# Performance work log

Hardware: AMD Instinct MI355X
Metric: run time of the kernel (lower is better)

## Reference

```python
import jax, jax.numpy as jnp
import numpy as np

N_FFT = 256
HOP = 64
HS = 126  # window hop in STFT frames (hard-coded in original)


def _stft(x):
    # torch.stft(center=True, pad_mode='reflect', window=None -> rectangular,
    # onesided=True, normalized=False). x: [B, N] -> [B, T, F] (time-major,
    # matching the module's permute(0,1,3,2)).
    pad = N_FFT // 2
    xp = jnp.pad(x, ((0, 0), (pad, pad)), mode='reflect')
    T = x.shape[-1] // HOP + 1
    idx = jnp.arange(T)[:, None] * HOP + jnp.arange(N_FFT)[None, :]  # [T, n_fft]
    frames = xp[:, idx]  # [B, T, n_fft]
    return jnp.fft.rfft(frames, axis=-1)  # [B, T, F=129]


def _spec_match(mix, aux):
    mixS = _stft(mix[:, 0, :])  # [B, Tm, F] complex
    auxS = _stft(aux[:, 0, :])  # [B, Ta, F] complex
    B, Tm, F = mixS.shape
    Ta = auxS.shape[1]
    length = (Ta - Tm) // HS
    pad = HS - (Ta - Tm) % HS
    auxS = jnp.pad(auxS, ((0, 0), (0, pad), (0, 0)))
    # All sliding windows at once: [B, W, Tm, F]
    W = length + 2
    widx = jnp.arange(W)[:, None] * HS + jnp.arange(Tm)[None, :]  # [W, Tm]
    wins = auxS[:, widx, :]  # [B, W, Tm, F]
    # Real part of complex cosine similarity, elementwise
    m = mixS[:, None]  # [B, 1, Tm, F]
    sim = (m.real * wins.real + m.imag * wins.imag) / (jnp.abs(m) * jnp.abs(wins))
    flat = sim.reshape(B, W, -1)
    n = flat.shape[-1]
    # torch.median = lower median; torch.median returns NaN if any NaN present
    srt = jnp.sort(flat, axis=-1)
    med = srt[..., (n - 1) // 2]
    med = jnp.where(jnp.isnan(flat).any(-1), -jnp.inf, med)
    best = jnp.argmax(med, axis=1)  # [B], first max like Python max()
    sel = jnp.take_along_axis(wins, best[:, None, None, None], axis=1)  # [B,1,Tm,F]
    return jnp.concatenate([sel.real, sel.imag], axis=1)  # [B, 2, Tm, F]


def setup_inputs() -> dict:
    key = jax.random.key(0)
    k1, k2 = jax.random.split(key)
    mix = jax.random.normal(k1, (8, 1, 65536), dtype=jnp.float32)
    aux = jax.random.normal(k2, (8, 1, 262144), dtype=jnp.float32)
    return {"mix": mix, "aux": aux}


def reference(mix, aux):
    return _spec_match(mix, aux)
```

## Files before the change

### kernel.cpp

```cpp
#include <hip/hip_runtime.h>
#include <math.h>

constexpr int NFFT  = 256;
constexpr int HOP   = 64;
constexpr int NBIN  = 129;
constexpr int NB    = 8;
constexpr int LMIX  = 65536;
constexpr int LAUX  = 262144;
constexpr int TM    = 1025;
constexpr int TA    = 4097;
constexpr int TROWS = 4175;
constexpr int HS    = 126;
constexpr int W     = 26;
constexpr int NJOBS = NB * W;
constexpr int NVAL  = TM * NBIN;
constexpr int KMED  = (NVAL - 1) / 2;
constexpr int CHUNKS = 8;
constexpr int NBA   = 1024;
constexpr int FPB   = 8;
constexpr int MIXBLKS = (TM + FPB - 1) / FPB;
constexpr int AUXBLKS = (TROWS + FPB - 1) / FPB;
constexpr int GFPB  = 4;
constexpr int GBLKS = (TM + GFPB - 1) / GFPB;

constexpr size_t MIXN_OFF  = 0;
constexpr size_t MIXN_BYTES = (size_t)NB * TM * NBIN * sizeof(float2);
constexpr size_t AUXN_OFF  = MIXN_OFF + MIXN_BYTES;
constexpr size_t AUXN_BYTES = (size_t)NB * TROWS * NBIN * sizeof(float2);
constexpr size_t HIST_OFF  = AUXN_OFF + AUXN_BYTES;
constexpr size_t HIST_BYTES = (size_t)NJOBS * CHUNKS * NBA * 4;
constexpr size_t CAND_OFF  = HIST_OFF + HIST_BYTES;
constexpr size_t CAND_BYTES = (size_t)NJOBS * NVAL * 4;
constexpr size_t NAN_OFF   = CAND_OFF + CAND_BYTES;
constexpr size_t NAN_BYTES = (size_t)NJOBS * CHUNKS * 4;
constexpr size_t NCAND_OFF = NAN_OFF + NAN_BYTES;
constexpr size_t SELBIN_OFF= NCAND_OFF + 832;
constexpr size_t KREM_OFF  = SELBIN_OFF + 832;
constexpr size_t MED_OFF   = KREM_OFF + 832;

constexpr float TWOPI_N = (float)(-2.0 * 3.14159265358979323846 / 256.0);

__device__ __forceinline__ float2 twiddle(int k) {
    float s, c;
    sincosf(TWOPI_N * (float)k, &s, &c);
    return make_float2(c, s);
}

__global__ void stft_all(const float* __restrict__ mix, const float* __restrict__ aux,
                         float2* __restrict__ mixN, float2* __restrict__ auxN,
                         unsigned* __restrict__ ncand)
{
    constexpr int NX = 64 * (FPB - 1) + NFFT;
    __shared__ float  xs[NX];
    __shared__ float2 Yl[FPB][16][16];
    __shared__ float2 tw256[256];
    __shared__ float2 cis16[16];

    const int tid  = threadIdx.x;
    const int wgid = blockIdx.x;
    const int b    = wgid & 7;
    const int t    = wgid >> 3;
    const bool isMix = t < MIXBLKS;
    const int f0 = (isMix ? t : t - MIXBLKS) * FPB;
    const int L       = isMix ? LMIX : LAUX;
    const int Tframes = isMix ? TM : TA;
    const int Trows   = isMix ? TM : TROWS;
    const float* x    = isMix ? mix : aux;
    float2* out       = isMix ? mixN : auxN;

    if (wgid == 0 && tid < NJOBS) ncand[tid] = 0u;

    tw256[tid] = twiddle(tid);
    if (tid < 16) cis16[tid] = twiddle(16 * tid);

    for (int i = tid; i < NX; i += 256) {
        int j = f0 * HOP + i - 128;
        if (j < 0) j = -j;
        if (j >= L) j = 2 * L - 2 - j;
        xs[i] = x[(size_t)b * L + j];
    }
    __syncthreads();

    const int n1 = (tid >> 4) & 15;
    const int r  = tid & 15;
    {
        float reA[FPB], imA[FPB];
        #pragma unroll
        for (int f = 0; f < FPB; ++f) { reA[f] = 0.f; imA[f] = 0.f; }
        int idx = 0;
        #pragma unroll
        for (int n2 = 0; n2 < 16; ++n2) {
            float2 tv = cis16[idx];
            #pragma unroll
            for (int f = 0; f < FPB; ++f) {
                float v = xs[f * HOP + n1 + 16 * n2];
                reA[f] = fmaf(v, tv.x, reA[f]);
                imA[f] = fmaf(v, tv.y, imA[f]);
            }
            idx = (idx + r) & 15;
        }
        #pragma unroll
        for (int f = 0; f < FPB; ++f) Yl[f][n1][r] = make_float2(reA[f], imA[f]);
    }
    __syncthreads();

    const float QNAN = __int_as_float(0x7FC00000);
    auto emit = [&](int fr, int k, float ar, float ai) {
        if (fr >= Trows) return;
        float2 o;
        if (fr < Tframes) {
            float inv = rsqrtf(ar * ar + ai * ai);
            o = make_float2(ar * inv, ai * inv);
        } else {
            o = make_float2(QNAN, QNAN);
        }
        out[((size_t)b * Trows + fr) * NBIN + k] = o;
    };

    #pragma unroll 1
    for (int p = 0; p < 2; ++p) {
        const int jjA = tid + 512 * p;
        const int jjB = jjA + 256;
        const int fA = jjA / NBIN, kA = jjA - fA * NBIN;
        const int fB = jjB / NBIN, kB = jjB - fB * NBIN;
        const float2 dkA = tw256[kA];
        const float2 dkB = tw256[kB];
        float trA = 1.f, tiA = 0.f, arA = 0.f, aiA = 0.f;
        float trB = 1.f, tiB = 0.f, arB = 0.f, aiB = 0.f;
        #pragma unroll
        for (int s = 0; s < 16; ++s) {
            float2 yA = Yl[fA][s][kA & 15];
            float2 yB = Yl[fB][s][kB & 15];
            arA = fmaf(trA, yA.x, arA); arA = fmaf(-tiA, yA.y, arA);
            aiA = fmaf(trA, yA.y, aiA); aiA = fmaf( tiA, yA.x, aiA);
            arB = fmaf(trB, yB.x, arB); arB = fmaf(-tiB, yB.y, arB);
            aiB = fmaf(trB, yB.y, aiB); aiB = fmaf( tiB, yB.x, aiB);
            float nrA = trA * dkA.x - tiA * dkA.y;
            tiA = fmaf(trA, dkA.y, tiA * dkA.x); trA = nrA;
            float nrB = trB * dkB.x - tiB * dkB.y;
            tiB = fmaf(trB, dkB.y, tiB * dkB.x); trB = nrB;
        }
        emit(f0 + fA, kA, arA, aiA);
        emit(f0 + fB, kB, arB, aiB);
    }
    if (tid < FPB * NBIN - 1024) {
        const int jj = 1024 + tid;
        const int f = jj / NBIN, k = jj - f * NBIN;
        const float2 dk = tw256[k];
        float tr = 1.f, ti = 0.f, ar = 0.f, ai = 0.f;
        #pragma unroll
        for (int s = 0; s < 16; ++s) {
            float2 y = Yl[f][s][k & 15];
            ar = fmaf(tr, y.x, ar); ar = fmaf(-ti, y.y, ar);
            ai = fmaf(tr, y.y, ai); ai = fmaf( ti, y.x, ai);
            float nr = tr * dk.x - ti * dk.y;
            ti = fmaf(tr, dk.y, ti * dk.x); tr = nr;
        }
        emit(f0 + f, k, ar, ai);
    }
}

__device__ __forceinline__ unsigned flip_key(float s) {
    unsigned u = __float_as_uint(s);
    return (u & 0x80000000u) ? ~u : (u | 0x80000000u);
}
__device__ __forceinline__ unsigned qbin(float s) {
    if (!(s == s)) return (unsigned)(NBA - 1);
    int bq = (int)floorf(fmaf(s, 512.f, 512.f));
    bq = max(0, min(NBA - 1, bq));
    return (unsigned)bq;
}

template<int PER>
__device__ __forceinline__ void rank_find(const unsigned (&bins)[PER], unsigned target,
                                          unsigned& out_bin, unsigned& out_rem)
{
    __shared__ unsigned wtot[4];
    __shared__ unsigned result[2];
    const int tid  = threadIdx.x;
    const int lane = tid & 63;
    const int wid  = tid >> 6;

    unsigned st = 0;
    #pragma unroll
    for (int i = 0; i < PER; ++i) st += bins[i];

    unsigned inc = st;
    #pragma unroll
    for (int d = 1; d < 64; d <<= 1) {
        unsigned v = __shfl_up(inc, d);
        if (lane >= d) inc += v;
    }
    if (lane == 63) wtot[wid] = inc;
    __syncthreads();

    unsigned wbase = 0;
    for (int wme = 0; wme < wid; ++wme) wbase += wtot[wme];
    unsigned ex = wbase + inc - st;
    if ((ex <= target) && (target < ex + st)) {
        unsigned cum = ex;
        #pragma unroll
        for (int i = 0; i < PER; ++i) {
            if (cum + bins[i] > target) {
                result[0] = (unsigned)(tid * PER + i);
                result[1] = target - cum;
                break;
            }
            cum += bins[i];
        }
    }
    __syncthreads();
    out_bin = result[0];
    out_rem = result[1];
}

__global__ void sim_hist(const float2* __restrict__ mixN, const float2* __restrict__ auxN,
                         unsigned* __restrict__ hist, unsigned* __restrict__ nanCnt)
{
    constexpr int NCOPY   = 4;
    constexpr int HSTRIDE = NBA + 1;
    __shared__ unsigned lh[NCOPY * HSTRIDE];
    __shared__ unsigned bnan;
    const int tid   = threadIdx.x;
    const int wgid  = blockIdx.x;
    const int b     = wgid & 7;
    const int rest  = wgid >> 3;
    const int w     = rest / CHUNKS;
    const int chunk = rest - w * CHUNKS;
    const int job   = b * W + w;
    unsigned* lhc = lh + ((tid >> 4) & (NCOPY - 1)) * HSTRIDE;

    for (int i = tid; i < NCOPY * HSTRIDE; i += 256) lh[i] = 0;
    if (tid == 0) bnan = 0;
    __syncthreads();

    unsigned localnan = 0;
    const float2* mrow = mixN + (size_t)b * TM * NBIN;
    const float2* arow = auxN + ((size_t)b * TROWS + (size_t)w * HS) * NBIN;

    const int pad = b & 1;
    const int lim = pad + ((NVAL - pad) & ~1);

    for (int i = pad + (chunk * 256 + tid) * 2; i < lim; i += CHUNKS * 512) {
        float4 mv = *reinterpret_cast<const float4*>(mrow + i);
        float4 av = *reinterpret_cast<const float4*>(arow + i);
        float s0 = fmaf(mv.x, av.x, mv.y * av.y);
        float s1 = fmaf(mv.z, av.z, mv.w * av.w);
        if (!(s0 == s0)) localnan++;
        if (!(s1 == s1)) localnan++;
        atomicAdd(&lhc[qbin(s0)], 1u);
        atomicAdd(&lhc[qbin(s1)], 1u);
    }
    if (chunk == 0 && tid == 0) {
        int ie = pad ? 0 : NVAL - 1;
        float2 m = mrow[ie];
        float2 a = arow[ie];
        float s = fmaf(m.x, a.x, m.y * a.y);
        if (!(s == s)) localnan++;
        atomicAdd(&lhc[qbin(s)], 1u);
    }
    if (localnan) atomicAdd(&bnan, localnan);
    __syncthreads();

    unsigned* gh = hist + ((size_t)job * CHUNKS + chunk) * NBA;
    for (int i = tid; i < NBA; i += 256)
        gh[i] = lh[i] + lh[HSTRIDE + i] + lh[2 * HSTRIDE + i] + lh[3 * HSTRIDE + i];
    if (tid == 0) nanCnt[job * CHUNKS + chunk] = bnan;
}

__global__ void scan_bins(const unsigned* __restrict__ hist, unsigned* __restrict__ selbin,
                          unsigned* __restrict__ krem)
{
    constexpr int PER = NBA / 256;
    const int tid  = threadIdx.x;
    const int wgid = blockIdx.x;
    const int job  = (wgid & 7) * W + (wgid >> 3);
    const unsigned* h = hist + (size_t)job * CHUNKS * NBA;

    unsigned bins[PER];
    #pragma unroll
    for (int i = 0; i < PER; ++i) {
        unsigned v = 0;
        int bin = tid * PER + i;
        #pragma unroll
        for (int c = 0; c < CHUNKS; ++c) v += h[(size_t)c * NBA + bin];
        bins[i] = v;
    }
    unsigned sb, rem;
    rank_find<PER>(bins, (unsigned)KMED, sb, rem);
    if (tid == 0) { selbin[job] = sb; krem[job] = rem; }
}

__global__ void sim_compact(const float2* __restrict__ mixN, const float2* __restrict__ auxN,
                            const unsigned* __restrict__ selbin, unsigned* __restrict__ cand,
                            unsigned* __restrict__ ncand)
{
    const int tid   = threadIdx.x;
    const int wgid  = blockIdx.x;
    const int b     = wgid & 7;
    const int rest  = wgid >> 3;
    const int w     = rest / CHUNKS;
    const int chunk = rest - w * CHUNKS;
    const int job   = b * W + w;
    const unsigned sb = selbin[job];

    unsigned* candj  = cand + (size_t)job * NVAL;
    unsigned* ncandj = ncand + job;
    const int lane = tid & 63;

    const float2* mrow = mixN + (size_t)b * TM * NBIN;
    const float2* arow = auxN + ((size_t)b * TROWS + (size_t)w * HS) * NBIN;

    const int pad = b & 1;
    const int lim = pad + ((NVAL - pad) & ~1);

    for (int i = pad + (chunk * 256 + tid) * 2; i < lim; i += CHUNKS * 512) {
        float4 mv = *reinterpret_cast<const float4*>(mrow + i);
        float4 av = *reinterpret_cast<const float4*>(arow + i);
        float sv[2];
        sv[0] = fmaf(mv.x, av.x, mv.y * av.y);
        sv[1] = fmaf(mv.z, av.z, mv.w * av.w);
        #pragma unroll
        for (int u = 0; u < 2; ++u) {
            bool pred = (qbin(sv[u]) == sb);
            unsigned long long m = __ballot(pred);
            if (m) {
                int leader = __ffsll(m) - 1;
                unsigned base = 0;
                if (lane == leader) base = atomicAdd(ncandj, (unsigned)__popcll(m));
                base = (unsigned)__shfl((int)base, leader);
                if (pred) candj[base + __popcll(m & ((1ull << lane) - 1ull))] = flip_key(sv[u]);
            }
        }
    }
    if (chunk == 0 && tid == 0) {
        int ie = pad ? 0 : NVAL - 1;
        float2 m = mrow[ie];
        float2 a = arow[ie];
        float s = fmaf(m.x, a.x, m.y * a.y);
        if (qbin(s) == sb) {
            unsigned idx = atomicAdd(ncandj, 1u);
            candj[idx] = flip_key(s);
        }
    }
}

__global__ void select_kernel(const unsigned* __restrict__ cand, const unsigned* __restrict__ ncand,
                              const unsigned* __restrict__ krem, const unsigned* __restrict__ nanCnt,
                              float* __restrict__ med)
{
    __shared__ unsigned h[2048];
    const int wgid = blockIdx.x;
    const int job  = (wgid & 7) * W + (wgid >> 3);
    const int tid  = threadIdx.x;
    const unsigned* c = cand + (size_t)job * NVAL;
    const unsigned n = ncand[job];
    unsigned pref = 0, tgt = krem[job];

    for (int ph = 0; ph < 3; ++ph) {
        for (int i = tid; i < 2048; i += 256) h[i] = 0;
        __syncthreads();
        for (unsigned i = tid; i < n; i += 256) {
            unsigned k = c[i];
            if (ph == 0) atomicAdd(&h[k >> 21], 1u);
            else if (ph == 1) { if ((k >> 21) == (pref >> 21)) atomicAdd(&h[(k >> 10) & 2047u], 1u); }
            else { if ((k >> 10) == (pref >> 10)) atomicAdd(&h[k & 1023u], 1u); }
        }
        __syncthreads();

        unsigned bins[8];
        #pragma unroll
        for (int i = 0; i < 8; ++i) bins[i] = h[tid * 8 + i];
        unsigned sb, rem;
        rank_find<8>(bins, tgt, sb, rem);

        if (ph == 0)      pref = sb << 21;
        else if (ph == 1) pref |= sb << 10;
        else              pref |= sb;
        tgt = rem;
        __syncthreads();
    }

    if (tid == 0) {
        unsigned nan = 0;
        #pragma unroll
        for (int c2 = 0; c2 < CHUNKS; ++c2) nan += nanCnt[job * CHUNKS + c2];
        unsigned key = pref;
        unsigned u = (key & 0x80000000u) ? (key ^ 0x80000000u) : ~key;
        med[job] = (nan > 0u) ? -INFINITY : __uint_as_float(u);
    }
}

__global__ void gather_stft(const float* __restrict__ x, const float* __restrict__ med,
                            float* __restrict__ out)
{
    constexpr int NX = 64 * (GFPB - 1) + NFFT;
    __shared__ float  xs[NX];
    __shared__ float2 Yl[GFPB][16][16];
    __shared__ float2 tw256[256];
    __shared__ float2 cis16[16];
    __shared__ int sh_best;

    const int tid  = threadIdx.x;
    const int wgid = blockIdx.x;
    const int b    = wgid & 7;
    const int t0   = (wgid >> 3) * GFPB;

    if (tid == 0) {
        float mx = -INFINITY; int bi = 0;
        for (int w = 0; w < W; ++w) {
            float v = med[b * W + w];
            if (v > mx) { mx = v; bi = w; }
        }
        sh_best = bi;
    }
    tw256[tid] = twiddle(tid);
    if (tid < 16) cis16[tid] = twiddle(16 * tid);
    __syncthreads();

    const int fr0 = sh_best * HS + t0;

    for (int i = tid; i < NX; i += 256) {
        int j = fr0 * HOP + i - 128;
        if (j < 0) j = -j;
        if (j >= LAUX) j = 2 * LAUX - 2 - j;
        j = max(0, min(LAUX - 1, j));
        xs[i] = x[(size_t)b * LAUX + j];
    }
    __syncthreads();

    const int n1 = (tid >> 4) & 15;
    const int r  = tid & 15;
    {
        float reA[GFPB], imA[GFPB];
        #pragma unroll
        for (int f = 0; f < GFPB; ++f) { reA[f] = 0.f; imA[f] = 0.f; }
        int idx = 0;
        #pragma unroll
        for (int n2 = 0; n2 < 16; ++n2) {
            float2 tv = cis16[idx];
            #pragma unroll
            for (int f = 0; f < GFPB; ++f) {
                float v = xs[f * HOP + n1 + 16 * n2];
                reA[f] = fmaf(v, tv.x, reA[f]);
                imA[f] = fmaf(v, tv.y, imA[f]);
            }
            idx = (idx + r) & 15;
        }
        #pragma unroll
        for (int f = 0; f < GFPB; ++f) Yl[f][n1][r] = make_float2(reA[f], imA[f]);
    }
    __syncthreads();

    auto dotask = [&](int jj) {
        const int f = jj / NBIN, k = jj - f * NBIN;
        const int tt = t0 + f;
        if (tt >= TM) return;
        float ar = 0.f, ai = 0.f;
        if (fr0 + f < TA) {
            const float2 dk = tw256[k];
            float tr = 1.f, ti = 0.f;
            #pragma unroll
            for (int s = 0; s < 16; ++s) {
                float2 y = Yl[f][s][k & 15];
                ar = fmaf(tr, y.x, ar); ar = fmaf(-ti, y.y, ar);
                ai = fmaf(tr, y.y, ai); ai = fmaf( ti, y.x, ai);
                float nr = tr * dk.x - ti * dk.y;
                ti = fmaf(tr, dk.y, ti * dk.x); tr = nr;
            }
        }
        size_t o = (size_t)tt * NBIN + k;
        out[(size_t)(b * 2 + 0) * NVAL + o] = ar;
        out[(size_t)(b * 2 + 1) * NVAL + o] = ai;
    };
    dotask(tid);
    dotask(tid + 256);
    if (tid < GFPB * NBIN - 512) dotask(512 + tid);
}

extern "C" void kernel_launch(void* const* d_in, const int* in_sizes, int n_in,
                              void* d_out, int out_size, void* d_ws, size_t ws_size,
                              hipStream_t stream)
{
    const float* mix = (const float*)d_in[0];
    const float* aux = (const float*)d_in[1];
    float* out = (float*)d_out;
    char* ws = (char*)d_ws;

    float2*   mixN = (float2*)(ws + MIXN_OFF);
    float2*   auxN = (float2*)(ws + AUXN_OFF);
    unsigned* hist = (unsigned*)(ws + HIST_OFF);
    unsigned* cand = (unsigned*)(ws + CAND_OFF);
    unsigned* nanC = (unsigned*)(ws + NAN_OFF);
    unsigned* ncand= (unsigned*)(ws + NCAND_OFF);
    unsigned* selb = (unsigned*)(ws + SELBIN_OFF);
    unsigned* krem = (unsigned*)(ws + KREM_OFF);
    float*    med  = (float*)(ws + MED_OFF);

    stft_all<<<(MIXBLKS + AUXBLKS) * NB, 256, 0, stream>>>(mix, aux, mixN, auxN, ncand);
    sim_hist<<<NJOBS * CHUNKS, 256, 0, stream>>>(mixN, auxN, hist, nanC);
    scan_bins<<<NJOBS, 256, 0, stream>>>(hist, selb, krem);
    sim_compact<<<NJOBS * CHUNKS, 256, 0, stream>>>(mixN, auxN, selb, cand, ncand);
    select_kernel<<<NJOBS, 256, 0, stream>>>(cand, ncand, krem, nanC, med);
    gather_stft<<<GBLKS * NB, 256, 0, stream>>>(aux, med, out);
}
```

Baseline: 122.9 us.

## Cache coarse bin bytes in histogram pass to skip recompute in compaction

The histogram pass now also writes one byte per similarity value holding the coarse bin (bin>>2). The compaction pass reads these bytes eight at a time, uses a SWAR zero-byte test to find possible matches, and only then loads the mix/aux spectra to recompute and check the exact bin. This replaces the full re-read of both complex spectra (16 bytes per element) with a 1-byte-per-element stream plus sparse gathers. It costs an extra byte-array write in sim_hist and adds scattered per-candidate atomics. The gather kernel also doubles frames per block and loops over tasks.

Measured after the change: 126.5 us. +2.9%, slower.

```diff
diff --git a/kernel.cpp b/kernel.cpp
--- a/kernel.cpp
+++ b/kernel.cpp
@@ -14,13 +14,14 @@
 constexpr int W     = 26;
 constexpr int NJOBS = NB * W;
 constexpr int NVAL  = TM * NBIN;
+constexpr int NVALB = 132232;
 constexpr int KMED  = (NVAL - 1) / 2;
 constexpr int CHUNKS = 8;
 constexpr int NBA   = 1024;
 constexpr int FPB   = 8;
 constexpr int MIXBLKS = (TM + FPB - 1) / FPB;
 constexpr int AUXBLKS = (TROWS + FPB - 1) / FPB;
-constexpr int GFPB  = 4;
+constexpr int GFPB  = 8;
 constexpr int GBLKS = (TM + GFPB - 1) / GFPB;
 
 constexpr size_t MIXN_OFF  = 0;
@@ -31,7 +32,9 @@
 constexpr size_t HIST_BYTES = (size_t)NJOBS * CHUNKS * NBA * 4;
 constexpr size_t CAND_OFF  = HIST_OFF + HIST_BYTES;
 constexpr size_t CAND_BYTES = (size_t)NJOBS * NVAL * 4;
-constexpr size_t NAN_OFF   = CAND_OFF + CAND_BYTES;
+constexpr size_t BYTES_OFF = CAND_OFF + CAND_BYTES;
+constexpr size_t BYTES_BYTES = (size_t)NJOBS * NVALB;
+constexpr size_t NAN_OFF   = BYTES_OFF + BYTES_BYTES;
 constexpr size_t NAN_BYTES = (size_t)NJOBS * CHUNKS * 4;
 constexpr size_t NCAND_OFF = NAN_OFF + NAN_BYTES;
 constexpr size_t SELBIN_OFF= NCAND_OFF + 832;
@@ -215,7 +218,8 @@
 }
 
 __global__ void sim_hist(const float2* __restrict__ mixN, const float2* __restrict__ auxN,
-                         unsigned* __restrict__ hist, unsigned* __restrict__ nanCnt)
+                         unsigned* __restrict__ hist, unsigned char* __restrict__ bytes,
+                         unsigned* __restrict__ nanCnt)
 {
     constexpr int NCOPY   = 4;
     constexpr int HSTRIDE = NBA + 1;
@@ -237,6 +241,7 @@
     unsigned localnan = 0;
     const float2* mrow = mixN + (size_t)b * TM * NBIN;
     const float2* arow = auxN + ((size_t)b * TROWS + (size_t)w * HS) * NBIN;
+    unsigned char* bj = bytes + (size_t)job * NVALB;
 
     const int pad = b & 1;
     const int lim = pad + ((NVAL - pad) & ~1);
@@ -248,8 +253,11 @@
         float s1 = fmaf(mv.z, av.z, mv.w * av.w);
         if (!(s0 == s0)) localnan++;
         if (!(s1 == s1)) localnan++;
-        atomicAdd(&lhc[qbin(s0)], 1u);
-        atomicAdd(&lhc[qbin(s1)], 1u);
+        unsigned b0 = qbin(s0), b1 = qbin(s1);
+        atomicAdd(&lhc[b0], 1u);
+        atomicAdd(&lhc[b1], 1u);
+        bj[i]     = (unsigned char)(b0 >> 2);
+        bj[i + 1] = (unsigned char)(b1 >> 2);
     }
     if (chunk == 0 && tid == 0) {
         int ie = pad ? 0 : NVAL - 1;
@@ -257,7 +265,9 @@
         float2 a = arow[ie];
         float s = fmaf(m.x, a.x, m.y * a.y);
         if (!(s == s)) localnan++;
-        atomicAdd(&lhc[qbin(s)], 1u);
+        unsigned be = qbin(s);
+        atomicAdd(&lhc[be], 1u);
+        bj[ie] = (unsigned char)(be >> 2);
     }
     if (localnan) atomicAdd(&bnan, localnan);
     __syncthreads();
@@ -292,6 +302,7 @@
 }
 
 __global__ void sim_compact(const float2* __restrict__ mixN, const float2* __restrict__ auxN,
+                            const unsigned char* __restrict__ bytes,
                             const unsigned* __restrict__ selbin, unsigned* __restrict__ cand,
                             unsigned* __restrict__ ncand)
 {
@@ -303,40 +314,36 @@
     const int chunk = rest - w * CHUNKS;
     const int job   = b * W + w;
     const unsigned sb = selbin[job];
+    const unsigned long long pat = 0x0101010101010101ULL * (unsigned long long)(sb >> 2);
 
     unsigned* candj  = cand + (size_t)job * NVAL;
     unsigned* ncandj = ncand + job;
-    const int lane = tid & 63;
-
     const float2* mrow = mixN + (size_t)b * TM * NBIN;
     const float2* arow = auxN + ((size_t)b * TROWS + (size_t)w * HS) * NBIN;
-
-    const int pad = b & 1;
-    const int lim = pad + ((NVAL - pad) & ~1);
-
-    for (int i = pad + (chunk * 256 + tid) * 2; i < lim; i += CHUNKS * 512) {
-        float4 mv = *reinterpret_cast<const float4*>(mrow + i);
-        float4 av = *reinterpret_cast<const float4*>(arow + i);
-        float sv[2];
-        sv[0] = fmaf(mv.x, av.x, mv.y * av.y);
-        sv[1] = fmaf(mv.z, av.z, mv.w * av.w);
-        #pragma unroll
-        for (int u = 0; u < 2; ++u) {
-            bool pred = (qbin(sv[u]) == sb);
-            unsigned long long m = __ballot(pred);
-            if (m) {
-                int leader = __ffsll(m) - 1;
-                unsigned base = 0;
-                if (lane == leader) base = atomicAdd(ncandj, (unsigned)__popcll(m));
-                base = (unsigned)__shfl((int)base, leader);
-                if (pred) candj[base + __popcll(m & ((1ull << lane) - 1ull))] = flip_key(sv[u]);
+    const unsigned long long* bj8 =
+        reinterpret_cast<const unsigned long long*>(bytes + (size_t)job * NVALB);
+
+    constexpr int NGRP = NVAL / 8;
+    for (int g = chunk * 256 + tid; g < NGRP; g += CHUNKS * 256) {
+        unsigned long long v = bj8[g];
+        unsigned long long x = v ^ pat;
+        unsigned long long z = (x - 0x0101010101010101ULL) & ~x & 0x8080808080808080ULL;
+        while (z) {
+            int e = g * 8 + ((__ffsll(z) - 1) >> 3);
+            z &= z - 1;
+            float2 m = mrow[e];
+            float2 a = arow[e];
+            float s = fmaf(m.x, a.x, m.y * a.y);
+            if (qbin(s) == sb) {
+                unsigned idx = atomicAdd(ncandj, 1u);
+                candj[idx] = flip_key(s);
             }
         }
     }
     if (chunk == 0 && tid == 0) {
-        int ie = pad ? 0 : NVAL - 1;
-        float2 m = mrow[ie];
-        float2 a = arow[ie];
+        int e = NVAL - 1;
+        float2 m = mrow[e];
+        float2 a = arow[e];
         float s = fmaf(m.x, a.x, m.y * a.y);
         if (qbin(s) == sb) {
             unsigned idx = atomicAdd(ncandj, 1u);
@@ -473,9 +480,12 @@
         out[(size_t)(b * 2 + 0) * NVAL + o] = ar;
         out[(size_t)(b * 2 + 1) * NVAL + o] = ai;
     };
-    dotask(tid);
-    dotask(tid + 256);
-    if (tid < GFPB * NBIN - 512) dotask(512 + tid);
+    #pragma unroll 1
+    for (int p = 0; p < 2; ++p) {
+        dotask(tid + 512 * p);
+        dotask(tid + 512 * p + 256);
+    }
+    if (tid < GFPB * NBIN - 1024) dotask(1024 + tid);
 }
 
 extern "C" void kernel_launch(void* const* d_in, const int* in_sizes, int n_in,
@@ -491,6 +501,7 @@
     float2*   auxN = (float2*)(ws + AUXN_OFF);
     unsigned* hist = (unsigned*)(ws + HIST_OFF);
     unsigned* cand = (unsigned*)(ws + CAND_OFF);
+    unsigned char* byt = (unsigned char*)(ws + BYTES_OFF);
     unsigned* nanC = (unsigned*)(ws + NAN_OFF);
     unsigned* ncand= (unsigned*)(ws + NCAND_OFF);
     unsigned* selb = (unsigned*)(ws + SELBIN_OFF);
@@ -498,9 +509,9 @@
     float*    med  = (float*)(ws + MED_OFF);
 
     stft_all<<<(MIXBLKS + AUXBLKS) * NB, 256, 0, stream>>>(mix, aux, mixN, auxN, ncand);
-    sim_hist<<<NJOBS * CHUNKS, 256, 0, stream>>>(mixN, auxN, hist, nanC);
+    sim_hist<<<NJOBS * CHUNKS, 256, 0, stream>>>(mixN, auxN, hist, byt, nanC);
     scan_bins<<<NJOBS, 256, 0, stream>>>(hist, selb, krem);
-    sim_compact<<<NJOBS * CHUNKS, 256, 0, stream>>>(mixN, auxN, selb, cand, ncand);
+    sim_compact<<<NJOBS * CHUNKS, 256, 0, stream>>>(mixN, auxN, byt, selb, cand, ncand);
     select_kernel<<<NJOBS, 256, 0, stream>>>(cand, ncand, krem, nanC, med);
     gather_stft<<<GBLKS * NB, 256, 0, stream>>>(aux, med, out);
 }
```
